# Performance work log

Measured on AMD Instinct MI355X. Metric: run time of the kernel, lower is better.

## Reference

```python
import jax, jax.numpy as jnp
import numpy as np

VARIANCE = (0.1, 0.2)
THRESHOLD = 0.5
NEG_POS = 3


def point_form(boxes):
    # (cx,cy,w,h) -> (xmin,ymin,xmax,ymax)
    return jnp.concatenate([boxes[:, :2] - boxes[:, 2:] / 2,
                            boxes[:, :2] + boxes[:, 2:] / 2], axis=1)


def jaccard(a, b):
    # a: [T,4] xyxy truths, b: [P,4] xyxy priors -> IoU [T,P]
    lt = jnp.maximum(a[:, None, :2], b[None, :, :2])
    rb = jnp.minimum(a[:, None, 2:], b[None, :, 2:])
    wh = jnp.clip(rb - lt, 0.0)
    inter = wh[..., 0] * wh[..., 1]
    area_a = ((a[:, 2] - a[:, 0]) * (a[:, 3] - a[:, 1]))[:, None]
    area_b = ((b[:, 2] - b[:, 0]) * (b[:, 3] - b[:, 1]))[None, :]
    return inter / (area_a + area_b - inter)


def encode(matched, priors):
    g_cxcy = (matched[:, :2] + matched[:, 2:]) / 2 - priors[:, :2]
    g_cxcy = g_cxcy / (VARIANCE[0] * priors[:, 2:])
    g_wh = jnp.log((matched[:, 2:] - matched[:, :2]) / priors[:, 2:]) / VARIANCE[1]
    return jnp.concatenate([g_cxcy, g_wh], axis=1)


def match_one(truths, priors):
    # SSD match for one image; labels are zeroed in BiBoxLoss -> binary conf {0,1}
    overlaps = jaccard(truths, point_form(priors))          # [T,P]
    best_prior_idx = jnp.argmax(overlaps, axis=1)           # [T]
    best_truth_overlap = jnp.max(overlaps, axis=0)          # [P]
    best_truth_idx = jnp.argmax(overlaps, axis=0)           # [P]
    best_truth_overlap = best_truth_overlap.at[best_prior_idx].set(2.0)
    best_truth_idx = best_truth_idx.at[best_prior_idx].set(
        jnp.arange(truths.shape[0]))
    matched = truths[best_truth_idx]                        # [P,4]
    conf = jnp.where(best_truth_overlap < THRESHOLD, 0, 1)  # [P] int
    loc = encode(matched, priors)
    return loc, conf


def bibox_loss(loc_data, conf_data, priors, targets):
    num, num_priors = loc_data.shape[0], loc_data.shape[1]
    truths = targets[..., :4]                               # [B,T,4]
    loc_t, conf_t = jax.vmap(lambda t: match_one(t, priors))(truths)

    pos = conf_t > 0                                        # [B,P]
    # smooth L1 (sum) over positive priors
    ad = jnp.abs(loc_data - loc_t)
    sl1 = jnp.where(ad < 1.0, 0.5 * ad * ad, ad - 0.5)
    loss_l = jnp.sum(sl1 * pos[..., None].astype(loc_data.dtype))

    # per-prior CE (logsumexp - gathered logit) for hard-negative mining
    lse = jax.nn.logsumexp(conf_data, axis=-1)              # [B,P]
    gathered = jnp.take_along_axis(conf_data, conf_t[..., None], axis=-1)[..., 0]
    loss_c_all = lse - gathered                             # [B,P]

    loss_c_mine = jnp.where(pos, 0.0, loss_c_all)
    loss_idx = jnp.argsort(-loss_c_mine, axis=1)
    idx_rank = jnp.argsort(loss_idx, axis=1)                # rank of each prior
    num_pos = jnp.sum(pos.astype(jnp.int32), axis=1, keepdims=True)  # [B,1]
    num_neg = jnp.minimum(NEG_POS * num_pos, num_priors - 1)
    neg = idx_rank < num_neg                                # [B,P]

    sel = pos | neg
    loss_c = jnp.sum(jnp.where(sel, loss_c_all, 0.0))

    N = jnp.sum(num_pos).astype(loc_data.dtype)
    return loss_l / N, loss_c / N


def setup_inputs() -> dict:
    key = jax.random.key(0)
    k1, k2, k3, k4, k5, k6 = jax.random.split(key, 6)
    B, P, T = 32, 65536, 16
    loc_data = jax.random.normal(k1, (B, P, 4), dtype=jnp.float32)
    conf_data = jax.random.normal(k2, (B, P, 2), dtype=jnp.float32)
    # priors: valid center-form boxes
    pc = 0.15 + 0.7 * jax.random.uniform(k3, (P, 2), dtype=jnp.float32)
    pwh = 0.05 + 0.25 * jax.random.uniform(k4, (P, 2), dtype=jnp.float32)
    priors = jnp.concatenate([pc, pwh], axis=1)
    # targets: valid corner-form boxes + dummy label column (zeroed by the loss)
    tc = 0.2 + 0.6 * jax.random.uniform(k5, (B, T, 2), dtype=jnp.float32)
    twh = 0.05 + 0.25 * jax.random.uniform(k6, (B, T, 2), dtype=jnp.float32)
    boxes = jnp.concatenate([tc - twh / 2, tc + twh / 2], axis=-1)
    targets = jnp.concatenate(
        [boxes, jnp.ones((B, T, 1), dtype=jnp.float32)], axis=-1)
    return {"loc_data": loc_data, "conf_data": conf_data,
            "priors": priors, "targets": targets}


def reference(loc_data, conf_data, priors, targets):
    return bibox_loss(loc_data, conf_data, priors, targets)
```

## Files before the change

kernel.cpp:

```cpp
#include <hip/hip_runtime.h>

#define NB_ 32
#define NP_ 65536
#define NT_ 16
#define HB 1024
#define HSCALE 128.0f
#define NBX 64

__device__ __forceinline__ float softplus_(float x) {
    return fmaxf(x, 0.0f) + __logf(1.0f + __expf(-fabsf(x)));
}

__device__ __forceinline__ float iou_fast(float tx0, float ty0, float tx1, float ty1, float ta,
                                          float bx0, float by0, float bx1, float by1, float ar) {
    float lx = fmaxf(tx0, bx0), ly = fmaxf(ty0, by0);
    float rx = fminf(tx1, bx1), ry = fminf(ty1, by1);
    float w = fmaxf(rx - lx, 0.0f), h = fmaxf(ry - ly, 0.0f);
    float inter = w * h;
    return __fdividef(inter, ta + ar - inter);
}

#define DPP_STEP(x, t, ctrl, rmask, bmask, OP)                                          \
    t = __builtin_amdgcn_update_dpp(0, (x), (ctrl), (rmask), (bmask), true); OP;

__device__ __forceinline__ unsigned wave_max_u32(unsigned v) {
    int x = (int)v, t;
    DPP_STEP(x, t, 0x111, 0xf, 0xf, x = ((unsigned)t > (unsigned)x) ? t : x)
    DPP_STEP(x, t, 0x112, 0xf, 0xf, x = ((unsigned)t > (unsigned)x) ? t : x)
    DPP_STEP(x, t, 0x114, 0xf, 0xe, x = ((unsigned)t > (unsigned)x) ? t : x)
    DPP_STEP(x, t, 0x118, 0xf, 0xc, x = ((unsigned)t > (unsigned)x) ? t : x)
    DPP_STEP(x, t, 0x142, 0xa, 0xf, x = ((unsigned)t > (unsigned)x) ? t : x)
    DPP_STEP(x, t, 0x143, 0xc, 0xf, x = ((unsigned)t > (unsigned)x) ? t : x)
    return (unsigned)x;
}

__device__ __forceinline__ float wave_sum_f32(float v) {
    int x = __float_as_int(v), t;
    float f;
    DPP_STEP(x, t, 0x111, 0xf, 0xf, f = __int_as_float(x) + __int_as_float(t); x = __float_as_int(f))
    DPP_STEP(x, t, 0x112, 0xf, 0xf, f = __int_as_float(x) + __int_as_float(t); x = __float_as_int(f))
    DPP_STEP(x, t, 0x114, 0xf, 0xe, f = __int_as_float(x) + __int_as_float(t); x = __float_as_int(f))
    DPP_STEP(x, t, 0x118, 0xf, 0xc, f = __int_as_float(x) + __int_as_float(t); x = __float_as_int(f))
    DPP_STEP(x, t, 0x142, 0xa, 0xf, f = __int_as_float(x) + __int_as_float(t); x = __float_as_int(f))
    DPP_STEP(x, t, 0x143, 0xc, 0xf, f = __int_as_float(x) + __int_as_float(t); x = __float_as_int(f))
    return __int_as_float(x);
}

__device__ __forceinline__ int wave_sum_i32(int v) {
    int x = v, t;
    DPP_STEP(x, t, 0x111, 0xf, 0xf, x = x + t)
    DPP_STEP(x, t, 0x112, 0xf, 0xf, x = x + t)
    DPP_STEP(x, t, 0x114, 0xf, 0xe, x = x + t)
    DPP_STEP(x, t, 0x118, 0xf, 0xc, x = x + t)
    DPP_STEP(x, t, 0x142, 0xa, 0xf, x = x + t)
    DPP_STEP(x, t, 0x143, 0xc, 0xf, x = x + t)
    return x;
}

__global__ void __launch_bounds__(256) mainK(
    const float* __restrict__ loc, const float* __restrict__ conf,
    const float* __restrict__ priors, const float* __restrict__ targets,
    unsigned short* __restrict__ gcnt, float* __restrict__ gsum,
    unsigned long long* __restrict__ bestPart,
    float* __restrict__ part_ll, float* __restrict__ part_pc, int* __restrict__ part_np,
    unsigned* __restrict__ ticket)
{
    const int bx = blockIdx.x, b = blockIdx.y, tid = threadIdx.x;

    __shared__ float4 trb[NT_];
    __shared__ float tra[NT_];
    __shared__ int hc[HB];
    __shared__ float hs[HB];
    __shared__ unsigned wkey[4][NT_], wp[4][NT_];
    __shared__ float sh_ll[4], sh_pc[4];
    __shared__ int sh_np[4];

    if (b == 0 && bx == 0 && tid == 0) *ticket = 0u;

    for (int i = tid; i < HB; i += 256) { hc[i] = 0; hs[i] = 0.0f; }
    if (tid < NT_) {
        const float* tp = targets + ((size_t)b * NT_ + tid) * 5;
        float x0 = tp[0], y0 = tp[1], x1 = tp[2], y1 = tp[3];
        trb[tid] = make_float4(x0, y0, x1, y1);
        tra[tid] = (x1 - x0) * (y1 - y0);
    }
    __syncthreads();

    const int pbase = bx * 1024 + tid;
    float pbx0[4], pby0[4], pbx1[4], pby1[4], par[4];
    float2 cxy[4];
#pragma unroll
    for (int i = 0; i < 4; i++) {
        float4 pr = ((const float4*)priors)[pbase + 256 * i];
        cxy[i] = ((const float2*)conf)[(size_t)b * NP_ + pbase + 256 * i];
        float hw = pr.z * 0.5f, hh = pr.w * 0.5f;
        pbx0[i] = pr.x - hw; pby0[i] = pr.y - hh;
        pbx1[i] = pr.x + hw; pby1[i] = pr.y + hh;
        par[i] = (pbx1[i] - pbx0[i]) * (pby1[i] - pby0[i]);
    }

    unsigned pkey[4] = {0u, 0u, 0u, 0u};
    unsigned tkey[NT_];
#pragma unroll
    for (int t = 0; t < NT_; t++) tkey[t] = 0u;

#pragma unroll
    for (int t = 0; t < NT_; t++) {
        float4 tb = trb[t];
        float ta = tra[t];
#pragma unroll
        for (int i = 0; i < 4; i++) {
            float iou = iou_fast(tb.x, tb.y, tb.z, tb.w, ta,
                                 pbx0[i], pby0[i], pbx1[i], pby1[i], par[i]);
            unsigned base = (__float_as_uint(iou) & 0xFFFFFFFCu) << 2;
            unsigned kt = base | (unsigned)(15 - t);
            unsigned kp = base | (unsigned)(15 - i);
            pkey[i] = (kt > pkey[i]) ? kt : pkey[i];
            tkey[t] = (kp > tkey[t]) ? kp : tkey[t];
        }
    }

    float ll_acc = 0.0f, pc_acc = 0.0f;
    int np_acc = 0;
#pragma unroll
    for (int i = 0; i < 4; i++) {
        int p = pbase + 256 * i;
        size_t bp = (size_t)b * NP_ + p;
        bool pos = (pkey[i] >= 0xFC000000u);
        float dd = cxy[i].y - cxy[i].x;
        float v = pos ? 0.0f : softplus_(dd);
        int bin = min(HB - 1, (int)(v * HSCALE));
        atomicAdd(&hc[bin], 1);
        atomicAdd(&hs[bin], v);
        if (pos) {
            np_acc++;
            pc_acc += softplus_(-dd);
            int t = 15 - (int)(pkey[i] & 15u);
            float4 tb = trb[t];
            float4 prv = ((const float4*)priors)[p];
            float gcx = ((tb.x + tb.z) * 0.5f - prv.x) / (0.1f * prv.z);
            float gcy = ((tb.y + tb.w) * 0.5f - prv.y) / (0.1f * prv.w);
            float gw = __logf((tb.z - tb.x) / prv.z) * 5.0f;
            float gh = __logf((tb.w - tb.y) / prv.w) * 5.0f;
            float4 ld = ((const float4*)loc)[bp];
            float d0 = fabsf(ld.x - gcx), d1 = fabsf(ld.y - gcy);
            float d2 = fabsf(ld.z - gw),  d3 = fabsf(ld.w - gh);
            ll_acc += (d0 < 1.0f) ? 0.5f * d0 * d0 : d0 - 0.5f;
            ll_acc += (d1 < 1.0f) ? 0.5f * d1 * d1 : d1 - 0.5f;
            ll_acc += (d2 < 1.0f) ? 0.5f * d2 * d2 : d2 - 0.5f;
            ll_acc += (d3 < 1.0f) ? 0.5f * d3 * d3 : d3 - 0.5f;
        }
    }

    const int wave = tid >> 6, lane = tid & 63;
#pragma unroll
    for (int t = 0; t < NT_; t++) {
        unsigned k = tkey[t];
        unsigned m = (unsigned)__builtin_amdgcn_readlane((int)wave_max_u32(k), 63);
        unsigned long long ball = __ballot(k == m);
        if (lane == 0) {
            int l = __ffsll((long long)ball) - 1;
            int ci = 15 - (int)(m & 15u);
            int p = bx * 1024 + ci * 256 + wave * 64 + l;
            wkey[wave][t] = m;
            wp[wave][t] = (unsigned)p;
        }
    }
    {
        float llw = wave_sum_f32(ll_acc);
        float pcw = wave_sum_f32(pc_acc);
        int npw = wave_sum_i32(np_acc);
        if (lane == 63) { sh_ll[wave] = llw; sh_pc[wave] = pcw; sh_np[wave] = npw; }
    }
    __syncthreads();

    if (tid < NT_) {
        unsigned bk = wkey[0][tid], bpv = wp[0][tid];
        for (int w = 1; w < 4; w++) {
            unsigned k2 = wkey[w][tid], p2 = wp[w][tid];
            if (k2 > bk || (k2 == bk && p2 < bpv)) { bk = k2; bpv = p2; }
        }
        unsigned long long pk = (((unsigned long long)bk) << 32) | (unsigned)(~bpv);
        bestPart[((size_t)b * NT_ + tid) * NBX + bx] = pk;
    }
    if (tid == 0) {
        part_ll[b * NBX + bx] = sh_ll[0] + sh_ll[1] + sh_ll[2] + sh_ll[3];
        part_pc[b * NBX + bx] = sh_pc[0] + sh_pc[1] + sh_pc[2] + sh_pc[3];
        part_np[b * NBX + bx] = sh_np[0] + sh_np[1] + sh_np[2] + sh_np[3];
    }
    unsigned short* gc = gcnt + ((size_t)(b * NBX + bx)) * HB;
    float* gs = gsum + ((size_t)(b * NBX + bx)) * HB;
    for (int i = tid; i < HB; i += 256) { gc[i] = (unsigned short)hc[i]; gs[i] = hs[i]; }
}

__global__ void __launch_bounds__(1024) finishK(
    const float* __restrict__ loc, const float* __restrict__ conf,
    const float* __restrict__ priors, const float* __restrict__ targets,
    const unsigned short* __restrict__ gcnt, const float* __restrict__ gsum,
    const unsigned long long* __restrict__ bestPart,
    const float* __restrict__ part_ll, const float* __restrict__ part_pc,
    const int* __restrict__ part_np,
    float* __restrict__ final_l, float* __restrict__ final_c, int* __restrict__ final_n,
    unsigned* __restrict__ ticket, float* __restrict__ out)
{
    const int b = blockIdx.x, tid = threadIdx.x;
    __shared__ int hc[HB];
    __shared__ float hs[HB];
    __shared__ float tr[NT_][5];
    __shared__ unsigned ps[NT_];
    __shared__ float s_dll, s_dpc;
    __shared__ int s_dnp;
    __shared__ unsigned ccnt[16];
    __shared__ float csm[16];
    __shared__ int s_last;

    if (tid == 0) { s_dll = 0.0f; s_dpc = 0.0f; s_dnp = 0; s_last = 0; }
    if (tid < NT_) {
        const float* tp = targets + ((size_t)b * NT_ + tid) * 5;
        float x0 = tp[0], y0 = tp[1], x1 = tp[2], y1 = tp[3];
        tr[tid][0] = x0; tr[tid][1] = y0; tr[tid][2] = x1; tr[tid][3] = y1;
        tr[tid][4] = (x1 - x0) * (y1 - y0);
    }
    {
        int i = tid;
        int c = 0; float s = 0.0f;
#pragma unroll
        for (int j = 0; j < NBX; j++) {
            c += (int)gcnt[((size_t)(b * NBX + j)) * HB + i];
            s += gsum[((size_t)(b * NBX + j)) * HB + i];
        }
        hc[i] = c; hs[i] = s;
    }
    if (tid < NT_) {
        unsigned long long v = bestPart[((size_t)b * NT_ + tid) * NBX];
        for (int j = 1; j < NBX; j++) {
            unsigned long long u = bestPart[((size_t)b * NT_ + tid) * NBX + j];
            if (u > v) v = u;
        }
        ps[tid] = ~((unsigned)(v & 0xffffffffULL));
    }
    __syncthreads();

    if (tid < NT_) {
        unsigned p = ps[tid];
        bool active = true;
        for (int u = tid + 1; u < NT_; u++)
            if (ps[u] == p) { active = false; break; }
        if (active) {
            float4 prv = ((const float4*)priors)[p];
            float hw = prv.z * 0.5f, hh = prv.w * 0.5f;
            float qx0 = prv.x - hw, qy0 = prv.y - hh;
            float qx1 = prv.x + hw, qy1 = prv.y + hh;
            float areab = (qx1 - qx0) * (qy1 - qy0);
            unsigned pk = 0u;
            for (int tt = 0; tt < NT_; tt++) {
                float iou = iou_fast(tr[tt][0], tr[tt][1], tr[tt][2], tr[tt][3], tr[tt][4],
                                     qx0, qy0, qx1, qy1, areab);
                unsigned cand = ((__float_as_uint(iou) & 0xFFFFFFFCu) << 2)
                              | (unsigned)(15 - tt);
                pk = (cand > pk) ? cand : pk;
            }
            bool pos0 = (pk >= 0xFC000000u);
            int t0 = 15 - (int)(pk & 15u);
            size_t bp = (size_t)b * NP_ + p;
            float2 cxy = ((const float2*)conf)[bp];
            float dd = cxy.y - cxy.x;
            float4 ld = ((const float4*)loc)[bp];

            auto sl1_of = [&](int tt) -> float {
                float tx0 = tr[tt][0], ty0 = tr[tt][1], tx1 = tr[tt][2], ty1 = tr[tt][3];
                float gcx = ((tx0 + tx1) * 0.5f - prv.x) / (0.1f * prv.z);
                float gcy = ((ty0 + ty1) * 0.5f - prv.y) / (0.1f * prv.w);
                float gw = __logf((tx1 - tx0) / prv.z) * 5.0f;
                float gh = __logf((ty1 - ty0) / prv.w) * 5.0f;
                float d0 = fabsf(ld.x - gcx), d1 = fabsf(ld.y - gcy);
                float d2 = fabsf(ld.z - gw),  d3 = fabsf(ld.w - gh);
                float s = (d0 < 1.0f) ? 0.5f * d0 * d0 : d0 - 0.5f;
                s += (d1 < 1.0f) ? 0.5f * d1 * d1 : d1 - 0.5f;
                s += (d2 < 1.0f) ? 0.5f * d2 * d2 : d2 - 0.5f;
                s += (d3 < 1.0f) ? 0.5f * d3 * d3 : d3 - 0.5f;
                return s;
            };
            float dll = sl1_of(tid) - (pos0 ? sl1_of(t0) : 0.0f);
            atomicAdd(&s_dll, dll);
            if (!pos0) {
                float v = softplus_(dd);
                int bin = min(HB - 1, (int)(v * HSCALE));
                atomicSub(&hc[bin], 1);
                atomicAdd(&hs[bin], -v);
                atomicAdd(&s_dpc, softplus_(-dd));
                atomicAdd(&s_dnp, 1);
            }
        }
    }
    __syncthreads();

    if (tid < 16) {
        unsigned cacc = 0; float sacc = 0.0f;
        for (int j = 0; j < 64; j++) { cacc += (unsigned)hc[tid * 64 + j]; sacc += hs[tid * 64 + j]; }
        ccnt[tid] = cacc; csm[tid] = sacc;
    }
    __syncthreads();

    if (tid == 0) {
        float sll = s_dll, spc = s_dpc;
        int n = s_dnp;
        for (int j = 0; j < NBX; j++) {
            sll += part_ll[b * NBX + j];
            spc += part_pc[b * NBX + j];
            n += part_np[b * NBX + j];
        }
        int K = 3 * n;
        if (K > NP_ - 1) K = NP_ - 1;
        float tk = 0.0f;
        if (K > 0) {
            unsigned need = (unsigned)K, cum = 0;
            float s = 0.0f;
            int cb = 15;
            for (; cb > 0; --cb) {
                if (cum + ccnt[cb] >= need) break;
                cum += ccnt[cb]; s += csm[cb];
            }
            int bin = cb * 64 + 63;
            for (; bin > cb * 64; --bin) {
                if (cum + (unsigned)hc[bin] >= need) break;
                cum += (unsigned)hc[bin]; s += hs[bin];
            }
            unsigned rem = need - cum;
            int cv = hc[bin];
            float avg = (cv > 0) ? __fdividef(hs[bin], (float)cv) : 0.0f;
            tk = s + (float)rem * avg;
        }
        final_l[b] = sll;
        final_c[b] = spc + tk;
        final_n[b] = n;
        __threadfence();
        unsigned old = atomicAdd(ticket, 1u);
        if (old == NB_ - 1) s_last = 1;
    }
    __syncthreads();

    if (s_last) {
        __threadfence();
        if (tid < 64) {
            float lv = 0.0f, cv = 0.0f;
            int nv = 0;
            if (tid < NB_) { lv = final_l[tid]; cv = final_c[tid]; nv = final_n[tid]; }
            for (int off = 32; off > 0; off >>= 1) {
                lv += __shfl_down(lv, off, 64);
                cv += __shfl_down(cv, off, 64);
                nv += __shfl_down(nv, off, 64);
            }
            if (tid == 0) {
                float fn = (float)nv;
                out[0] = lv / fn;
                out[1] = cv / fn;
            }
        }
    }
}

extern "C" void kernel_launch(void* const* d_in, const int* in_sizes, int n_in,
                              void* d_out, int out_size, void* d_ws, size_t ws_size,
                              hipStream_t stream) {
    const float* loc = (const float*)d_in[0];
    const float* conf = (const float*)d_in[1];
    const float* priors = (const float*)d_in[2];
    const float* targets = (const float*)d_in[3];
    float* out = (float*)d_out;

    char* w = (char*)d_ws;
    unsigned short* gcnt = (unsigned short*)w;
    float* gsum = (float*)(w + (4u << 20));
    char* acc = w + (12u << 20);
    unsigned long long* bestPart = (unsigned long long*)acc;
    float* part_ll = (float*)(acc + 262144);
    float* part_pc = (float*)(acc + 262144 + 8192);
    int* part_np   = (int*)(acc + 262144 + 16384);
    float* final_l = (float*)(acc + 262144 + 24576);
    float* final_c = (float*)(acc + 262144 + 24704);
    int* final_n   = (int*)(acc + 262144 + 24832);
    unsigned* ticket = (unsigned*)(acc + 262144 + 24960);

    mainK<<<dim3(NBX, NB_), 256, 0, stream>>>(loc, conf, priors, targets,
                                              gcnt, gsum, bestPart,
                                              part_ll, part_pc, part_np, ticket);
    finishK<<<NB_, 1024, 0, stream>>>(loc, conf, priors, targets, gcnt, gsum, bestPart,
                                      part_ll, part_pc, part_np,
                                      final_l, final_c, final_n, ticket, out);
}
```

Baseline: 140.6 us.

## Fuse finish kernel into main kernel via per-image last-block ticket

Removes the separate finishK launch. Each image's last-arriving block, detected through a per-image atomic ticket, now merges the histograms, fixes up the forced matches, selects the top-k and does the final cross-image reduction. A memset resets the tickets before the launch. This saves one kernel launch and the gap between the two kernels, but the merge now runs on a 256-thread block instead of 1024 threads, which serializes the histogram reduction more.

Result: slower. 385.1 us (+173.8%).

```diff
diff --git a/kernel.cpp b/kernel.cpp
--- a/kernel.cpp
+++ b/kernel.cpp
@@ -63,7 +63,9 @@
     unsigned short* __restrict__ gcnt, float* __restrict__ gsum,
     unsigned long long* __restrict__ bestPart,
     float* __restrict__ part_ll, float* __restrict__ part_pc, int* __restrict__ part_np,
-    unsigned* __restrict__ ticket)
+    float* __restrict__ final_l, float* __restrict__ final_c, int* __restrict__ final_n,
+    unsigned* __restrict__ ticketB, unsigned* __restrict__ ticket2,
+    float* __restrict__ out)
 {
     const int bx = blockIdx.x, b = blockIdx.y, tid = threadIdx.x;
 
@@ -74,8 +76,12 @@
     __shared__ unsigned wkey[4][NT_], wp[4][NT_];
     __shared__ float sh_ll[4], sh_pc[4];
     __shared__ int sh_np[4];
-
-    if (b == 0 && bx == 0 && tid == 0) *ticket = 0u;
+    __shared__ unsigned s_old;
+    __shared__ unsigned ps[NT_];
+    __shared__ float s_dll, s_dpc, s_sll, s_spc;
+    __shared__ int s_dnp, s_sn, s_last;
+    __shared__ unsigned ccnt[16];
+    __shared__ float csm[16];
 
     for (int i = tid; i < HB; i += 256) { hc[i] = 0; hs[i] = 0.0f; }
     if (tid < NT_) {
@@ -188,43 +194,23 @@
         part_pc[b * NBX + bx] = sh_pc[0] + sh_pc[1] + sh_pc[2] + sh_pc[3];
         part_np[b * NBX + bx] = sh_np[0] + sh_np[1] + sh_np[2] + sh_np[3];
     }
-    unsigned short* gc = gcnt + ((size_t)(b * NBX + bx)) * HB;
-    float* gs = gsum + ((size_t)(b * NBX + bx)) * HB;
-    for (int i = tid; i < HB; i += 256) { gc[i] = (unsigned short)hc[i]; gs[i] = hs[i]; }
-}
-
-__global__ void __launch_bounds__(1024) finishK(
-    const float* __restrict__ loc, const float* __restrict__ conf,
-    const float* __restrict__ priors, const float* __restrict__ targets,
-    const unsigned short* __restrict__ gcnt, const float* __restrict__ gsum,
-    const unsigned long long* __restrict__ bestPart,
-    const float* __restrict__ part_ll, const float* __restrict__ part_pc,
-    const int* __restrict__ part_np,
-    float* __restrict__ final_l, float* __restrict__ final_c, int* __restrict__ final_n,
-    unsigned* __restrict__ ticket, float* __restrict__ out)
-{
-    const int b = blockIdx.x, tid = threadIdx.x;
-    __shared__ int hc[HB];
-    __shared__ float hs[HB];
-    __shared__ float tr[NT_][5];
-    __shared__ unsigned ps[NT_];
-    __shared__ float s_dll, s_dpc;
-    __shared__ int s_dnp;
-    __shared__ unsigned ccnt[16];
-    __shared__ float csm[16];
-    __shared__ int s_last;
+    {
+        unsigned short* gc = gcnt + ((size_t)(b * NBX + bx)) * HB;
+        float* gs = gsum + ((size_t)(b * NBX + bx)) * HB;
+        for (int i = tid; i < HB; i += 256) { gc[i] = (unsigned short)hc[i]; gs[i] = hs[i]; }
+    }
+
+    __threadfence();
+    if (tid == 0) s_old = atomicAdd(&ticketB[b], 1u);
+    __syncthreads();
+    if (s_old != NBX - 1) return;
+
+    __threadfence();
 
     if (tid == 0) { s_dll = 0.0f; s_dpc = 0.0f; s_dnp = 0; s_last = 0; }
-    if (tid < NT_) {
-        const float* tp = targets + ((size_t)b * NT_ + tid) * 5;
-        float x0 = tp[0], y0 = tp[1], x1 = tp[2], y1 = tp[3];
-        tr[tid][0] = x0; tr[tid][1] = y0; tr[tid][2] = x1; tr[tid][3] = y1;
-        tr[tid][4] = (x1 - x0) * (y1 - y0);
-    }
-    {
-        int i = tid;
+    for (int i = tid; i < HB; i += 256) {
         int c = 0; float s = 0.0f;
-#pragma unroll
+#pragma unroll 8
         for (int j = 0; j < NBX; j++) {
             c += (int)gcnt[((size_t)(b * NBX + j)) * HB + i];
             s += gsum[((size_t)(b * NBX + j)) * HB + i];
@@ -238,6 +224,13 @@
             if (u > v) v = u;
         }
         ps[tid] = ~((unsigned)(v & 0xffffffffULL));
+    }
+    if (tid < 64) {
+        float lv = part_ll[b * NBX + tid];
+        float pv = part_pc[b * NBX + tid];
+        int nv = part_np[b * NBX + tid];
+        lv = wave_sum_f32(lv); pv = wave_sum_f32(pv); nv = wave_sum_i32(nv);
+        if (tid == 63) { s_sll = lv; s_spc = pv; s_sn = nv; }
     }
     __syncthreads();
 
@@ -254,7 +247,8 @@
             float areab = (qx1 - qx0) * (qy1 - qy0);
             unsigned pk = 0u;
             for (int tt = 0; tt < NT_; tt++) {
-                float iou = iou_fast(tr[tt][0], tr[tt][1], tr[tt][2], tr[tt][3], tr[tt][4],
+                float4 tb = trb[tt];
+                float iou = iou_fast(tb.x, tb.y, tb.z, tb.w, tra[tt],
                                      qx0, qy0, qx1, qy1, areab);
                 unsigned cand = ((__float_as_uint(iou) & 0xFFFFFFFCu) << 2)
                               | (unsigned)(15 - tt);
@@ -263,16 +257,16 @@
             bool pos0 = (pk >= 0xFC000000u);
             int t0 = 15 - (int)(pk & 15u);
             size_t bp = (size_t)b * NP_ + p;
-            float2 cxy = ((const float2*)conf)[bp];
-            float dd = cxy.y - cxy.x;
+            float2 cxyf = ((const float2*)conf)[bp];
+            float dd = cxyf.y - cxyf.x;
             float4 ld = ((const float4*)loc)[bp];
 
             auto sl1_of = [&](int tt) -> float {
-                float tx0 = tr[tt][0], ty0 = tr[tt][1], tx1 = tr[tt][2], ty1 = tr[tt][3];
-                float gcx = ((tx0 + tx1) * 0.5f - prv.x) / (0.1f * prv.z);
-                float gcy = ((ty0 + ty1) * 0.5f - prv.y) / (0.1f * prv.w);
-                float gw = __logf((tx1 - tx0) / prv.z) * 5.0f;
-                float gh = __logf((ty1 - ty0) / prv.w) * 5.0f;
+                float4 tb = trb[tt];
+                float gcx = ((tb.x + tb.z) * 0.5f - prv.x) / (0.1f * prv.z);
+                float gcy = ((tb.y + tb.w) * 0.5f - prv.y) / (0.1f * prv.w);
+                float gw = __logf((tb.z - tb.x) / prv.z) * 5.0f;
+                float gh = __logf((tb.w - tb.y) / prv.w) * 5.0f;
                 float d0 = fabsf(ld.x - gcx), d1 = fabsf(ld.y - gcy);
                 float d2 = fabsf(ld.z - gw),  d3 = fabsf(ld.w - gh);
                 float s = (d0 < 1.0f) ? 0.5f * d0 * d0 : d0 - 0.5f;
@@ -303,13 +297,9 @@
     __syncthreads();
 
     if (tid == 0) {
-        float sll = s_dll, spc = s_dpc;
-        int n = s_dnp;
-        for (int j = 0; j < NBX; j++) {
-            sll += part_ll[b * NBX + j];
-            spc += part_pc[b * NBX + j];
-            n += part_np[b * NBX + j];
-        }
+        float sll = s_sll + s_dll;
+        float spc = s_spc + s_dpc;
+        int n = s_sn + s_dnp;
         int K = 3 * n;
         if (K > NP_ - 1) K = NP_ - 1;
         float tk = 0.0f;
@@ -335,7 +325,7 @@
         final_c[b] = spc + tk;
         final_n[b] = n;
         __threadfence();
-        unsigned old = atomicAdd(ticket, 1u);
+        unsigned old = atomicAdd(ticket2, 1u);
         if (old == NB_ - 1) s_last = 1;
     }
     __syncthreads();
@@ -380,12 +370,14 @@
     float* final_l = (float*)(acc + 262144 + 24576);
     float* final_c = (float*)(acc + 262144 + 24704);
     int* final_n   = (int*)(acc + 262144 + 24832);
-    unsigned* ticket = (unsigned*)(acc + 262144 + 24960);
+    unsigned* ticketB = (unsigned*)(acc + 262144 + 24960);
+    unsigned* ticket2 = (unsigned*)(acc + 262144 + 25088);
+
+    hipMemsetAsync((void*)ticketB, 0, 256, stream);
 
     mainK<<<dim3(NBX, NB_), 256, 0, stream>>>(loc, conf, priors, targets,
                                               gcnt, gsum, bestPart,
-                                              part_ll, part_pc, part_np, ticket);
-    finishK<<<NB_, 1024, 0, stream>>>(loc, conf, priors, targets, gcnt, gsum, bestPart,
-                                      part_ll, part_pc, part_np,
-                                      final_l, final_c, final_n, ticket, out);
-}
+                                              part_ll, part_pc, part_np,
+                                              final_l, final_c, final_n,
+                                              ticketB, ticket2, out);
+}
```
